# Performance work log

Measured on AMD Instinct MI355X. Metric: run time of the kernel, lower is better.

## Reference

```python
import jax, jax.numpy as jnp
import numpy as np

D_MODEL = 1024
NUM_HEADS = 16


def setup_inputs() -> dict:
    key = jax.random.key(0)
    ks = jax.random.split(key, 5)
    B, S, D = 2, 2048, D_MODEL
    scale = 1.0 / np.sqrt(D)
    return {
        "x": jax.random.normal(ks[0], (B, S, D), dtype=jnp.float32),
        "q_proj_weight": jax.random.normal(ks[1], (D, D), dtype=jnp.float32) * scale,
        "k_proj_weight": jax.random.normal(ks[2], (D, D), dtype=jnp.float32) * scale,
        "v_proj_weight": jax.random.normal(ks[3], (D, D), dtype=jnp.float32) * scale,
        "o_proj_weight": jax.random.normal(ks[4], (D, D), dtype=jnp.float32) * scale,
    }


def _attn(x, qw, kw, vw, ow, num_heads):
    B, S, D = x.shape
    d_k = D // num_heads
    q = x @ qw.T  # [B,S,D]
    k = x @ kw.T
    v = x @ vw.T
    # split heads: [B, H, S, d_k]
    q = q.reshape(B, S, num_heads, d_k).transpose(0, 2, 1, 3)
    k = k.reshape(B, S, num_heads, d_k).transpose(0, 2, 1, 3)
    v = v.reshape(B, S, num_heads, d_k).transpose(0, 2, 1, 3)
    scores = jnp.einsum('bhqd,bhkd->bhqk', q, k) / jnp.sqrt(jnp.asarray(d_k, x.dtype))
    causal = jnp.tril(jnp.ones((S, S), dtype=bool))  # [S,S]
    scores = jnp.where(causal[None, None], scores, jnp.asarray(-jnp.inf, x.dtype))
    attn = jax.nn.softmax(scores, axis=-1)
    out = jnp.einsum('bhqk,bhkd->bhqd', attn, v)  # [B,H,S,d_k]
    out = out.transpose(0, 2, 1, 3).reshape(B, S, D)
    return out @ ow.T


def reference(x, q_proj_weight, k_proj_weight, v_proj_weight, o_proj_weight):
    return _attn(x, q_proj_weight, k_proj_weight, v_proj_weight, o_proj_weight, NUM_HEADS)
```

## Files before the change

kernel.cpp:

```cpp
#include <hip/hip_runtime.h>

typedef __attribute__((ext_vector_type(8))) short short8;
typedef __attribute__((ext_vector_type(4))) float f32x4;

#define MFMA(a,b,c) __builtin_amdgcn_mfma_f32_16x16x32_bf16((a),(b),(c),0,0,0)

#define B_  2
#define S_  2048
#define D_  1024
#define H_  16
#define DK  64
#define KDIM 1024

typedef unsigned int u32;
typedef __attribute__((address_space(1))) const u32 gu32;
typedef __attribute__((address_space(3))) u32 lu32;

__device__ __forceinline__ void gll16(const unsigned short* g, unsigned short* l){
  __builtin_amdgcn_global_load_lds((gu32*)g, (lu32*)l, 16, 0, 0);
}

__device__ __forceinline__ unsigned short f2bf(float f){
  unsigned int u = __float_as_uint(f);
  u += 0x7fffu + ((u >> 16) & 1u);
  return (unsigned short)(u >> 16);
}

__device__ __forceinline__ u32 pkbf(float lo, float hi){
  u32 a = __float_as_uint(lo) + 0x8000u;
  u32 b = __float_as_uint(hi) + 0x8000u;
  return __builtin_amdgcn_perm(b, a, 0x07060302u);
}

__global__ void cvt_all(const float* __restrict__ x,  const float* __restrict__ qw,
                        const float* __restrict__ kw, const float* __restrict__ vw,
                        const float* __restrict__ ow,
                        unsigned short* __restrict__ xb,  unsigned short* __restrict__ wqb,
                        unsigned short* __restrict__ wkb, unsigned short* __restrict__ wvb,
                        unsigned short* __restrict__ wob,
                        int n4x, int n4w){
  int i = blockIdx.x * 256 + threadIdx.x;
  const float* src; unsigned short* dst; int n4;
  switch (blockIdx.y) {
    case 0:  src = x;  dst = xb;  n4 = n4x; break;
    case 1:  src = qw; dst = wqb; n4 = n4w; break;
    case 2:  src = kw; dst = wkb; n4 = n4w; break;
    case 3:  src = vw; dst = wvb; n4 = n4w; break;
    default: src = ow; dst = wob; n4 = n4w; break;
  }
  if (i >= n4) return;
  float4 f = reinterpret_cast<const float4*>(src)[i];
  ushort4 u;
  u.x = f2bf(f.x); u.y = f2bf(f.y); u.z = f2bf(f.z); u.w = f2bf(f.w);
  reinterpret_cast<ushort4*>(dst)[i] = u;
}

__global__ __launch_bounds__(256) void gemm_qkv(
    const unsigned short* __restrict__ X,
    const unsigned short* __restrict__ Wq,
    const unsigned short* __restrict__ Wk,
    const unsigned short* __restrict__ Wv,
    unsigned short* __restrict__ Qo,
    unsigned short* __restrict__ Ko,
    unsigned short* __restrict__ Vo)
{
  const int z = blockIdx.z;
  const unsigned short* __restrict__ W = (z == 0) ? Wq : (z == 1) ? Wk : Wv;
  const int n0 = blockIdx.x * 64;
  const int m0 = blockIdx.y * 128;

  __shared__ unsigned short As0[128 * 32];
  __shared__ unsigned short As1[128 * 32];
  __shared__ unsigned short Bs0[64 * 32];
  __shared__ unsigned short Bs1[64 * 32];

  const int tid  = threadIdx.x;
  const int wid  = tid >> 6, lane = tid & 63;
  const int wm   = (wid >> 1) * 64, wn = (wid & 1) * 32;
  const int lr   = lane & 15, lk = (lane >> 4) * 8;

  const int srow = lane >> 2;
  const int scol = (lane & 3) * 8;
  const unsigned short* gA = X + (size_t)(m0 + wid * 32 + srow) * KDIM + scol;
  const unsigned short* gB = W + (size_t)(n0 + wid * 16 + srow) * KDIM + scol;
  unsigned short* lA0 = &As0[(wid * 32) * 32];
  unsigned short* lA1 = &As1[(wid * 32) * 32];
  unsigned short* lB0 = &Bs0[(wid * 16) * 32];
  unsigned short* lB1 = &Bs1[(wid * 16) * 32];

  f32x4 acc[4][2];
  const f32x4 z4 = {0.f, 0.f, 0.f, 0.f};
  for (int i = 0; i < 4; i++)
    for (int j = 0; j < 2; j++) acc[i][j] = z4;

  for (int k0 = 0; k0 < KDIM; k0 += 64) {
    __syncthreads();
    gll16(gA + k0,                  lA0);
    gll16(gA + 16 * KDIM + k0,      lA0 + 16 * 32);
    gll16(gA + k0 + 32,             lA1);
    gll16(gA + 16 * KDIM + k0 + 32, lA1 + 16 * 32);
    gll16(gB + k0,                  lB0);
    gll16(gB + k0 + 32,             lB1);
    __syncthreads();

    short8 a[4], b[2];
    for (int i = 0; i < 4; i++) a[i] = *(const short8*)&As0[(wm + i * 16 + lr) * 32 + lk];
    for (int j = 0; j < 2; j++) b[j] = *(const short8*)&Bs0[(wn + j * 16 + lr) * 32 + lk];
    if (z == 2) {
      for (int i = 0; i < 4; i++)
        for (int j = 0; j < 2; j++)
          acc[i][j] = MFMA(b[j], a[i], acc[i][j]);
    } else {
      for (int i = 0; i < 4; i++)
        for (int j = 0; j < 2; j++)
          acc[i][j] = MFMA(a[i], b[j], acc[i][j]);
    }
    for (int i = 0; i < 4; i++) a[i] = *(const short8*)&As1[(wm + i * 16 + lr) * 32 + lk];
    for (int j = 0; j < 2; j++) b[j] = *(const short8*)&Bs1[(wn + j * 16 + lr) * 32 + lk];
    if (z == 2) {
      for (int i = 0; i < 4; i++)
        for (int j = 0; j < 2; j++)
          acc[i][j] = MFMA(b[j], a[i], acc[i][j]);
    } else {
      for (int i = 0; i < 4; i++)
        for (int j = 0; j < 2; j++)
          acc[i][j] = MFMA(a[i], b[j], acc[i][j]);
    }
  }

  const int rbase = (lane >> 4) * 4;
  if (z == 2) {
    for (int i = 0; i < 4; i++)
      for (int j = 0; j < 2; j++)
        for (int r = 0; r < 4; r++) {
          int dfull = n0 + wn + j * 16 + rbase + r;
          int sfull = m0 + wm + i * 16 + lr;
          int h = dfull >> 6, d = dfull & 63;
          int bb = sfull >> 11, s = sfull & 2047;
          Vo[(((bb * H_ + h) * DK) + d) * S_ + s] = f2bf(acc[i][j][r]);
        }
  } else {
    for (int i = 0; i < 4; i++)
      for (int j = 0; j < 2; j++)
        for (int r = 0; r < 4; r++) {
          int m = m0 + wm + i * 16 + rbase + r;
          int n = n0 + wn + j * 16 + lr;
          float v = acc[i][j][r];
          int bb = m >> 11, s = m & 2047, h = n >> 6, d = n & 63;
          if (z == 0) {
            v *= 0.18033688f;
            Qo[(((bb * H_ + h) * S_) + s) * DK + d] = f2bf(v);
          } else {
            Ko[(((bb * H_ + h) * S_) + s) * DK + d] = f2bf(v);
          }
        }
  }
}

__global__ __launch_bounds__(512, 4) void attn(
    const unsigned short* __restrict__ Q,
    const unsigned short* __restrict__ K,
    const unsigned short* __restrict__ V,
    unsigned short* __restrict__ O)
{
  const int h = blockIdx.y, b = blockIdx.z;
  const int qt = b ? (15 - blockIdx.x) : blockIdx.x;

  const unsigned short* __restrict__ Qh = Q + (size_t)((b * H_ + h) * S_) * DK;
  const unsigned short* __restrict__ Kh = K + (size_t)((b * H_ + h) * S_) * DK;
  const unsigned short* __restrict__ Vh = V + (size_t)((b * H_ + h) * DK) * S_;

  __shared__ unsigned short Ks[64][72];
  __shared__ unsigned short Vs[64][72];
  __shared__ unsigned short Ps[8][16][72];

  const int tid = threadIdx.x, wid = tid >> 6, lane = tid & 63;
  const int lr = lane & 15, lk = (lane >> 4) * 8;
  const int row4 = (lane >> 4) * 4;
  const int q0 = qt * 128;
  const int qcol = q0 + wid * 16 + lr;
  const int qwmin = q0 + wid * 16;
  const int qwmax = qwmin + 15;
  const int lrow = tid >> 3, lcol = (tid & 7) * 8;

  const short ONE = (short)0x3F80;
  const short8 ones = {ONE, ONE, ONE, ONE, ONE, ONE, ONE, ONE};

  short8 qf[2];
  qf[0] = *(const short8*)&Qh[(q0 + wid * 16 + lr) * DK + lk];
  qf[1] = *(const short8*)&Qh[(q0 + wid * 16 + lr) * DK + 32 + lk];

  const f32x4 z4 = {0.f, 0.f, 0.f, 0.f};
  f32x4 o[4];
  for (int i = 0; i < 4; i++) o[i] = z4;
  f32x4 rs = z4;

  const int kt_end = 2 * qt + 2;

  uint4 kr, vr;
  kr = *(const uint4*)&Kh[lrow * DK + lcol];
  vr = *(const uint4*)&Vh[lrow * S_ + lcol];

  for (int kt = 0; kt < kt_end; kt++) {
    const int k0 = kt * 64;
    __syncthreads();
    *(uint4*)&Ks[lrow][lcol] = kr;
    *(uint4*)&Vs[lrow][lcol] = vr;
    __syncthreads();

    if (kt + 1 < kt_end) {
      const int kn = k0 + 64;
      kr = *(const uint4*)&Kh[(kn + lrow) * DK + lcol];
      vr = *(const uint4*)&Vh[lrow * S_ + kn + lcol];
    }

    if (k0 <= qwmax) {
      f32x4 sc[4];
      for (int nt = 0; nt < 4; nt++) {
        short8 kb0 = *(const short8*)&Ks[nt * 16 + lr][lk];
        short8 kb1 = *(const short8*)&Ks[nt * 16 + lr][32 + lk];
        f32x4 s = MFMA(kb0, qf[0], z4);
        sc[nt] = MFMA(kb1, qf[1], s);
      }

      if (k0 + 63 > qwmin) {
        for (int nt = 0; nt < 4; nt++) {
          int kg = k0 + nt * 16 + row4;
          for (int r = 0; r < 4; r++)
            if (kg + r > qcol) sc[nt][r] = -INFINITY;
        }
      }

      for (int nt = 0; nt < 4; nt++) {
        float p0 = __builtin_amdgcn_exp2f(sc[nt][0]);
        float p1 = __builtin_amdgcn_exp2f(sc[nt][1]);
        float p2 = __builtin_amdgcn_exp2f(sc[nt][2]);
        float p3 = __builtin_amdgcn_exp2f(sc[nt][3]);
        uint2 pk;
        pk.x = pkbf(p0, p1);
        pk.y = pkbf(p2, p3);
        *(uint2*)&Ps[wid][lr][nt * 16 + row4] = pk;
      }

      short8 pf0 = *(const short8*)&Ps[wid][lr][lk];
      short8 pf1 = *(const short8*)&Ps[wid][lr][32 + lk];

      rs = MFMA(ones, pf0, rs);
      rs = MFMA(ones, pf1, rs);

      for (int dt = 0; dt < 4; dt++) {
        short8 vb0 = *(const short8*)&Vs[dt * 16 + lr][lk];
        short8 vb1 = *(const short8*)&Vs[dt * 16 + lr][32 + lk];
        o[dt] = MFMA(vb0, pf0, o[dt]);
        o[dt] = MFMA(vb1, pf1, o[dt]);
      }
    }
  }

  const float inv = 1.0f / rs[0];

  const int srow = q0 + wid * 16 + lr;
  for (int dt = 0; dt < 4; dt++) {
    uint2 pk;
    pk.x = pkbf(o[dt][0] * inv, o[dt][1] * inv);
    pk.y = pkbf(o[dt][2] * inv, o[dt][3] * inv);
    *(uint2*)&O[(size_t)(b * S_ + srow) * D_ + h * DK + dt * 16 + row4] = pk;
  }
}

__global__ __launch_bounds__(256) void gemm_oproj(
    const unsigned short* __restrict__ A,
    const unsigned short* __restrict__ W,
    float* __restrict__ out)
{
  const int n0 = blockIdx.x * 64;
  const int m0 = blockIdx.y * 128;

  __shared__ unsigned short As0[128 * 32];
  __shared__ unsigned short As1[128 * 32];
  __shared__ unsigned short Bs0[64 * 32];
  __shared__ unsigned short Bs1[64 * 32];

  const int tid  = threadIdx.x;
  const int wid  = tid >> 6, lane = tid & 63;
  const int wm   = (wid >> 1) * 64, wn = (wid & 1) * 32;
  const int lr   = lane & 15, lk = (lane >> 4) * 8;

  const int srow = lane >> 2;
  const int scol = (lane & 3) * 8;
  const unsigned short* gA = A + (size_t)(m0 + wid * 32 + srow) * KDIM + scol;
  const unsigned short* gB = W + (size_t)(n0 + wid * 16 + srow) * KDIM + scol;
  unsigned short* lA0 = &As0[(wid * 32) * 32];
  unsigned short* lA1 = &As1[(wid * 32) * 32];
  unsigned short* lB0 = &Bs0[(wid * 16) * 32];
  unsigned short* lB1 = &Bs1[(wid * 16) * 32];

  f32x4 acc[4][2];
  const f32x4 z4 = {0.f, 0.f, 0.f, 0.f};
  for (int i = 0; i < 4; i++)
    for (int j = 0; j < 2; j++) acc[i][j] = z4;

  for (int k0 = 0; k0 < KDIM; k0 += 64) {
    __syncthreads();
    gll16(gA + k0,                  lA0);
    gll16(gA + 16 * KDIM + k0,      lA0 + 16 * 32);
    gll16(gA + k0 + 32,             lA1);
    gll16(gA + 16 * KDIM + k0 + 32, lA1 + 16 * 32);
    gll16(gB + k0,                  lB0);
    gll16(gB + k0 + 32,             lB1);
    __syncthreads();

    short8 a[4], b[2];
    for (int i = 0; i < 4; i++) a[i] = *(const short8*)&As0[(wm + i * 16 + lr) * 32 + lk];
    for (int j = 0; j < 2; j++) b[j] = *(const short8*)&Bs0[(wn + j * 16 + lr) * 32 + lk];
    for (int i = 0; i < 4; i++)
      for (int j = 0; j < 2; j++)
        acc[i][j] = MFMA(a[i], b[j], acc[i][j]);
    for (int i = 0; i < 4; i++) a[i] = *(const short8*)&As1[(wm + i * 16 + lr) * 32 + lk];
    for (int j = 0; j < 2; j++) b[j] = *(const short8*)&Bs1[(wn + j * 16 + lr) * 32 + lk];
    for (int i = 0; i < 4; i++)
      for (int j = 0; j < 2; j++)
        acc[i][j] = MFMA(a[i], b[j], acc[i][j]);
  }

  const int rbase = (lane >> 4) * 4;
  for (int i = 0; i < 4; i++)
    for (int j = 0; j < 2; j++)
      for (int r = 0; r < 4; r++) {
        int m = m0 + wm + i * 16 + rbase + r;
        int n = n0 + wn + j * 16 + lr;
        out[(size_t)m * D_ + n] = acc[i][j][r];
      }
}

extern "C" void kernel_launch(void* const* d_in, const int* in_sizes, int n_in,
                              void* d_out, int out_size, void* d_ws, size_t ws_size,
                              hipStream_t stream) {
  const float* x  = (const float*)d_in[0];
  const float* qw = (const float*)d_in[1];
  const float* kw = (const float*)d_in[2];
  const float* vw = (const float*)d_in[3];
  const float* ow = (const float*)d_in[4];
  float* out = (float*)d_out;

  char* ws = (char*)d_ws;
  size_t off = 0;
  auto alloc = [&](size_t bytes) -> void* {
    void* p = ws + off;
    off += (bytes + 255) & ~(size_t)255;
    return p;
  };
  const size_t XN = (size_t)B_ * S_ * D_;
  const size_t WN = (size_t)D_ * D_;
  unsigned short* xb  = (unsigned short*)alloc(XN * 2);
  unsigned short* wqb = (unsigned short*)alloc(WN * 2);
  unsigned short* wkb = (unsigned short*)alloc(WN * 2);
  unsigned short* wvb = (unsigned short*)alloc(WN * 2);
  unsigned short* wob = (unsigned short*)alloc(WN * 2);
  unsigned short* Qb  = (unsigned short*)alloc(XN * 2);
  unsigned short* Kb  = (unsigned short*)alloc(XN * 2);
  unsigned short* Vb  = (unsigned short*)alloc(XN * 2);
  unsigned short* Ob  = (unsigned short*)alloc(XN * 2);

  cvt_all<<<dim3((XN / 4 + 255) / 256, 5), dim3(256), 0, stream>>>(
      x, qw, kw, vw, ow, xb, wqb, wkb, wvb, wob, (int)(XN / 4), (int)(WN / 4));

  gemm_qkv<<<dim3(D_ / 64, (B_ * S_) / 128, 3), dim3(256), 0, stream>>>(
      xb, wqb, wkb, wvb, Qb, Kb, Vb);

  attn<<<dim3(S_ / 128, H_, B_), dim3(512), 0, stream>>>(Qb, Kb, Vb, Ob);

  gemm_oproj<<<dim3(D_ / 64, (B_ * S_) / 128), dim3(256), 0, stream>>>(Ob, wob, out);
}
```

Before: 177.1 us.

## Double-buffer LDS loads in GEMMs and attention with async global-to-LDS copies

The QKV and output-projection GEMMs now split each K-step into two halves. The load of the next half into the other LDS buffer is issued before computing on the current half, so global-to-LDS copies overlap MFMA work instead of waiting behind a barrier. The attention kernel swaps its register-staged K/V prefetch for direct global_load_lds into double-buffered LDS tiles. It also adds an XOR-like swizzle in place of padding to avoid bank conflicts. This relies on the barrier implicitly waiting for outstanding async LDS loads, which is risky if the compiler does not insert vmcnt waits.

```diff
diff --git a/kernel.cpp b/kernel.cpp
--- a/kernel.cpp
+++ b/kernel.cpp
@@ -93,19 +93,10 @@
   for (int i = 0; i < 4; i++)
     for (int j = 0; j < 2; j++) acc[i][j] = z4;
 
-  for (int k0 = 0; k0 < KDIM; k0 += 64) {
-    __syncthreads();
-    gll16(gA + k0,                  lA0);
-    gll16(gA + 16 * KDIM + k0,      lA0 + 16 * 32);
-    gll16(gA + k0 + 32,             lA1);
-    gll16(gA + 16 * KDIM + k0 + 32, lA1 + 16 * 32);
-    gll16(gB + k0,                  lB0);
-    gll16(gB + k0 + 32,             lB1);
-    __syncthreads();
-
+  auto compute = [&](const unsigned short* AS, const unsigned short* BS){
     short8 a[4], b[2];
-    for (int i = 0; i < 4; i++) a[i] = *(const short8*)&As0[(wm + i * 16 + lr) * 32 + lk];
-    for (int j = 0; j < 2; j++) b[j] = *(const short8*)&Bs0[(wn + j * 16 + lr) * 32 + lk];
+    for (int i = 0; i < 4; i++) a[i] = *(const short8*)&AS[(wm + i * 16 + lr) * 32 + lk];
+    for (int j = 0; j < 2; j++) b[j] = *(const short8*)&BS[(wn + j * 16 + lr) * 32 + lk];
     if (z == 2) {
       for (int i = 0; i < 4; i++)
         for (int j = 0; j < 2; j++)
@@ -115,17 +106,29 @@
         for (int j = 0; j < 2; j++)
           acc[i][j] = MFMA(a[i], b[j], acc[i][j]);
     }
-    for (int i = 0; i < 4; i++) a[i] = *(const short8*)&As1[(wm + i * 16 + lr) * 32 + lk];
-    for (int j = 0; j < 2; j++) b[j] = *(const short8*)&Bs1[(wn + j * 16 + lr) * 32 + lk];
-    if (z == 2) {
-      for (int i = 0; i < 4; i++)
-        for (int j = 0; j < 2; j++)
-          acc[i][j] = MFMA(b[j], a[i], acc[i][j]);
-    } else {
-      for (int i = 0; i < 4; i++)
-        for (int j = 0; j < 2; j++)
-          acc[i][j] = MFMA(a[i], b[j], acc[i][j]);
-    }
+  };
+
+  gll16(gA,             lA0);
+  gll16(gA + 16 * KDIM, lA0 + 16 * 32);
+  gll16(gB,             lB0);
+
+  for (int k0 = 0; k0 < KDIM; k0 += 64) {
+    __syncthreads();
+    {
+      const int kn = k0 + 32;
+      gll16(gA + kn,             lA1);
+      gll16(gA + 16 * KDIM + kn, lA1 + 16 * 32);
+      gll16(gB + kn,             lB1);
+    }
+    compute(As0, Bs0);
+    __syncthreads();
+    if (k0 + 64 < KDIM) {
+      const int kn = k0 + 64;
+      gll16(gA + kn,             lA0);
+      gll16(gA + 16 * KDIM + kn, lA0 + 16 * 32);
+      gll16(gB + kn,             lB0);
+    }
+    compute(As1, Bs1);
   }
 
   const int rbase = (lane >> 4) * 4;
@@ -170,18 +173,34 @@
   const unsigned short* __restrict__ Kh = K + (size_t)((b * H_ + h) * S_) * DK;
   const unsigned short* __restrict__ Vh = V + (size_t)((b * H_ + h) * DK) * S_;
 
-  __shared__ unsigned short Ks[64][72];
-  __shared__ unsigned short Vs[64][72];
+  __shared__ unsigned short Ks0[64 * 64];
+  __shared__ unsigned short Ks1[64 * 64];
+  __shared__ unsigned short Vs0[64 * 64];
+  __shared__ unsigned short Vs1[64 * 64];
   __shared__ unsigned short Ps[8][16][72];
 
   const int tid = threadIdx.x, wid = tid >> 6, lane = tid & 63;
-  const int lr = lane & 15, lk = (lane >> 4) * 8;
+  const int lr = lane & 15;
   const int row4 = (lane >> 4) * 4;
   const int q0 = qt * 128;
   const int qcol = q0 + wid * 16 + lr;
   const int qwmin = q0 + wid * 16;
   const int qwmax = qwmin + 15;
-  const int lrow = tid >> 3, lcol = (tid & 7) * 8;
+  const int lk = (lane >> 4) * 8;
+
+  const int pc0 = (((lane >> 4) + lr) & 7) * 8;
+  const int pc1 = (((lane >> 4) + 4 + lr) & 7) * 8;
+
+  const int sr8 = lane >> 3;
+  const int sc8 = lane & 7;
+  const int sg  = (sc8 - sr8) & 7;
+  const int stRow = wid * 8 + sr8;
+  const unsigned short* gK = Kh + (size_t)stRow * DK + sg * 8;
+  const unsigned short* gV = Vh + (size_t)stRow * S_ + sg * 8;
+  unsigned short* lK0 = &Ks0[wid * 8 * 64];
+  unsigned short* lK1 = &Ks1[wid * 8 * 64];
+  unsigned short* lV0 = &Vs0[wid * 8 * 64];
+  unsigned short* lV1 = &Vs1[wid * 8 * 64];
 
   const short ONE = (short)0x3F80;
   const short8 ones = {ONE, ONE, ONE, ONE, ONE, ONE, ONE, ONE};
@@ -195,66 +214,63 @@
   for (int i = 0; i < 4; i++) o[i] = z4;
   f32x4 rs = z4;
 
+  auto tile = [&](int k0, const unsigned short* KS, const unsigned short* VS){
+    if (k0 > qwmax) return;
+    f32x4 sc[4];
+    for (int nt = 0; nt < 4; nt++) {
+      short8 kb0 = *(const short8*)&KS[(nt * 16 + lr) * 64 + pc0];
+      short8 kb1 = *(const short8*)&KS[(nt * 16 + lr) * 64 + pc1];
+      f32x4 s = MFMA(kb0, qf[0], z4);
+      sc[nt] = MFMA(kb1, qf[1], s);
+    }
+    if (k0 + 63 > qwmin) {
+      for (int nt = 0; nt < 4; nt++) {
+        int kg = k0 + nt * 16 + row4;
+        for (int r = 0; r < 4; r++)
+          if (kg + r > qcol) sc[nt][r] = -INFINITY;
+      }
+    }
+    for (int nt = 0; nt < 4; nt++) {
+      float p0 = __builtin_amdgcn_exp2f(sc[nt][0]);
+      float p1 = __builtin_amdgcn_exp2f(sc[nt][1]);
+      float p2 = __builtin_amdgcn_exp2f(sc[nt][2]);
+      float p3 = __builtin_amdgcn_exp2f(sc[nt][3]);
+      uint2 pk;
+      pk.x = pkbf(p0, p1);
+      pk.y = pkbf(p2, p3);
+      *(uint2*)&Ps[wid][lr][nt * 16 + row4] = pk;
+    }
+    short8 pf0 = *(const short8*)&Ps[wid][lr][lk];
+    short8 pf1 = *(const short8*)&Ps[wid][lr][32 + lk];
+    rs = MFMA(ones, pf0, rs);
+    rs = MFMA(ones, pf1, rs);
+    for (int dt = 0; dt < 4; dt++) {
+      short8 vb0 = *(const short8*)&VS[(dt * 16 + lr) * 64 + pc0];
+      short8 vb1 = *(const short8*)&VS[(dt * 16 + lr) * 64 + pc1];
+      o[dt] = MFMA(vb0, pf0, o[dt]);
+      o[dt] = MFMA(vb1, pf1, o[dt]);
+    }
+  };
+
   const int kt_end = 2 * qt + 2;
 
-  uint4 kr, vr;
-  kr = *(const uint4*)&Kh[lrow * DK + lcol];
-  vr = *(const uint4*)&Vh[lrow * S_ + lcol];
-
-  for (int kt = 0; kt < kt_end; kt++) {
+  gll16(gK, lK0);
+  gll16(gV, lV0);
+
+  for (int kt = 0; kt < kt_end; kt += 2) {
     const int k0 = kt * 64;
     __syncthreads();
-    *(uint4*)&Ks[lrow][lcol] = kr;
-    *(uint4*)&Vs[lrow][lcol] = vr;
-    __syncthreads();
-
-    if (kt + 1 < kt_end) {
-      const int kn = k0 + 64;
-      kr = *(const uint4*)&Kh[(kn + lrow) * DK + lcol];
-      vr = *(const uint4*)&Vh[lrow * S_ + kn + lcol];
-    }
-
-    if (k0 <= qwmax) {
-      f32x4 sc[4];
-      for (int nt = 0; nt < 4; nt++) {
-        short8 kb0 = *(const short8*)&Ks[nt * 16 + lr][lk];
-        short8 kb1 = *(const short8*)&Ks[nt * 16 + lr][32 + lk];
-        f32x4 s = MFMA(kb0, qf[0], z4);
-        sc[nt] = MFMA(kb1, qf[1], s);
-      }
-
-      if (k0 + 63 > qwmin) {
-        for (int nt = 0; nt < 4; nt++) {
-          int kg = k0 + nt * 16 + row4;
-          for (int r = 0; r < 4; r++)
-            if (kg + r > qcol) sc[nt][r] = -INFINITY;
-        }
-      }
-
-      for (int nt = 0; nt < 4; nt++) {
-        float p0 = __builtin_amdgcn_exp2f(sc[nt][0]);
-        float p1 = __builtin_amdgcn_exp2f(sc[nt][1]);
-        float p2 = __builtin_amdgcn_exp2f(sc[nt][2]);
-        float p3 = __builtin_amdgcn_exp2f(sc[nt][3]);
-        uint2 pk;
-        pk.x = pkbf(p0, p1);
-        pk.y = pkbf(p2, p3);
-        *(uint2*)&Ps[wid][lr][nt * 16 + row4] = pk;
-      }
-
-      short8 pf0 = *(const short8*)&Ps[wid][lr][lk];
-      short8 pf1 = *(const short8*)&Ps[wid][lr][32 + lk];
-
-      rs = MFMA(ones, pf0, rs);
-      rs = MFMA(ones, pf1, rs);
-
-      for (int dt = 0; dt < 4; dt++) {
-        short8 vb0 = *(const short8*)&Vs[dt * 16 + lr][lk];
-        short8 vb1 = *(const short8*)&Vs[dt * 16 + lr][32 + lk];
-        o[dt] = MFMA(vb0, pf0, o[dt]);
-        o[dt] = MFMA(vb1, pf1, o[dt]);
-      }
-    }
+    {
+      gll16(gK + (size_t)(k0 + 64) * DK, lK1);
+      gll16(gV + (k0 + 64),              lV1);
+    }
+    tile(k0, Ks0, Vs0);
+    __syncthreads();
+    if (kt + 2 < kt_end) {
+      gll16(gK + (size_t)(k0 + 128) * DK, lK0);
+      gll16(gV + (k0 + 128),              lV0);
+    }
+    tile(k0 + 64, Ks1, Vs1);
   }
 
   const float inv = 1.0f / rs[0];
@@ -300,27 +316,36 @@
   for (int i = 0; i < 4; i++)
     for (int j = 0; j < 2; j++) acc[i][j] = z4;
 
-  for (int k0 = 0; k0 < KDIM; k0 += 64) {
-    __syncthreads();
-    gll16(gA + k0,                  lA0);
-    gll16(gA + 16 * KDIM + k0,      lA0 + 16 * 32);
-    gll16(gA + k0 + 32,             lA1);
-    gll16(gA + 16 * KDIM + k0 + 32, lA1 + 16 * 32);
-    gll16(gB + k0,                  lB0);
-    gll16(gB + k0 + 32,             lB1);
-    __syncthreads();
-
+  auto compute = [&](const unsigned short* AS, const unsigned short* BS){
     short8 a[4], b[2];
-    for (int i = 0; i < 4; i++) a[i] = *(const short8*)&As0[(wm + i * 16 + lr) * 32 + lk];
-    for (int j = 0; j < 2; j++) b[j] = *(const short8*)&Bs0[(wn + j * 16 + lr) * 32 + lk];
+    for (int i = 0; i < 4; i++) a[i] = *(const short8*)&AS[(wm + i * 16 + lr) * 32 + lk];
+    for (int j = 0; j < 2; j++) b[j] = *(const short8*)&BS[(wn + j * 16 + lr) * 32 + lk];
     for (int i = 0; i < 4; i++)
       for (int j = 0; j < 2; j++)
         acc[i][j] = MFMA(a[i], b[j], acc[i][j]);
-    for (int i = 0; i < 4; i++) a[i] = *(const short8*)&As1[(wm + i * 16 + lr) * 32 + lk];
-    for (int j = 0; j < 2; j++) b[j] = *(const short8*)&Bs1[(wn + j * 16 + lr) * 32 + lk];
-    for (int i = 0; i < 4; i++)
-      for (int j = 0; j < 2; j++)
-        acc[i][j] = MFMA(a[i], b[j], acc[i][j]);
+  };
+
+  gll16(gA,             lA0);
+  gll16(gA + 16 * KDIM, lA0 + 16 * 32);
+  gll16(gB,             lB0);
+
+  for (int k0 = 0; k0 < KDIM; k0 += 64) {
+    __syncthreads();
+    {
+      const int kn = k0 + 32;
+      gll16(gA + kn,             lA1);
+      gll16(gA + 16 * KDIM + kn, lA1 + 16 * 32);
+      gll16(gB + kn,             lB1);
+    }
+    compute(As0, Bs0);
+    __syncthreads();
+    if (k0 + 64 < KDIM) {
+      const int kn = k0 + 64;
+      gll16(gA + kn,             lA0);
+      gll16(gA + 16 * KDIM + kn, lA0 + 16 * 32);
+      gll16(gB + kn,             lB0);
+    }
+    compute(As1, Bs1);
   }
 
   const int rbase = (lane >> 4) * 4;
```

Result: no change. 177.4 us (+0.2%).

## Double-buffer attention K/V tiles with direct global-to-LDS loads and swizzled layout

Applied to the files above, without the earlier changes.

The attention kernel used to stage K/V tiles through registers and needed two barriers per tile. It now issues global_load_lds directly into two LDS buffers and processes tiles in pairs, so the next tile's copy overlaps compute with one barrier per tile. The padded 72-column LDS rows are replaced by an unpadded 64-column layout with an XOR-style chunk rotation to avoid bank conflicts. Correctness relies on the barrier implicitly waiting for the async LDS loads, which is a synchronisation risk.

```diff
diff --git a/kernel.cpp b/kernel.cpp
--- a/kernel.cpp
+++ b/kernel.cpp
@@ -170,18 +170,34 @@
   const unsigned short* __restrict__ Kh = K + (size_t)((b * H_ + h) * S_) * DK;
   const unsigned short* __restrict__ Vh = V + (size_t)((b * H_ + h) * DK) * S_;
 
-  __shared__ unsigned short Ks[64][72];
-  __shared__ unsigned short Vs[64][72];
+  __shared__ unsigned short Ks0[64 * 64];
+  __shared__ unsigned short Ks1[64 * 64];
+  __shared__ unsigned short Vs0[64 * 64];
+  __shared__ unsigned short Vs1[64 * 64];
   __shared__ unsigned short Ps[8][16][72];
 
   const int tid = threadIdx.x, wid = tid >> 6, lane = tid & 63;
-  const int lr = lane & 15, lk = (lane >> 4) * 8;
+  const int lr = lane & 15;
   const int row4 = (lane >> 4) * 4;
   const int q0 = qt * 128;
   const int qcol = q0 + wid * 16 + lr;
   const int qwmin = q0 + wid * 16;
   const int qwmax = qwmin + 15;
-  const int lrow = tid >> 3, lcol = (tid & 7) * 8;
+  const int lk = (lane >> 4) * 8;
+
+  const int pc0 = (((lane >> 4) + lr) & 7) * 8;
+  const int pc1 = (((lane >> 4) + 4 + lr) & 7) * 8;
+
+  const int sr8 = lane >> 3;
+  const int sc8 = lane & 7;
+  const int sg  = (sc8 - sr8) & 7;
+  const int stRow = wid * 8 + sr8;
+  const unsigned short* gK = Kh + (size_t)stRow * DK + sg * 8;
+  const unsigned short* gV = Vh + (size_t)stRow * S_ + sg * 8;
+  unsigned short* lK0 = &Ks0[wid * 8 * 64];
+  unsigned short* lK1 = &Ks1[wid * 8 * 64];
+  unsigned short* lV0 = &Vs0[wid * 8 * 64];
+  unsigned short* lV1 = &Vs1[wid * 8 * 64];
 
   const short ONE = (short)0x3F80;
   const short8 ones = {ONE, ONE, ONE, ONE, ONE, ONE, ONE, ONE};
@@ -195,66 +211,63 @@
   for (int i = 0; i < 4; i++) o[i] = z4;
   f32x4 rs = z4;
 
+  auto tile = [&](int k0, const unsigned short* KS, const unsigned short* VS){
+    if (k0 > qwmax) return;
+    f32x4 sc[4];
+    for (int nt = 0; nt < 4; nt++) {
+      short8 kb0 = *(const short8*)&KS[(nt * 16 + lr) * 64 + pc0];
+      short8 kb1 = *(const short8*)&KS[(nt * 16 + lr) * 64 + pc1];
+      f32x4 s = MFMA(kb0, qf[0], z4);
+      sc[nt] = MFMA(kb1, qf[1], s);
+    }
+    if (k0 + 63 > qwmin) {
+      for (int nt = 0; nt < 4; nt++) {
+        int kg = k0 + nt * 16 + row4;
+        for (int r = 0; r < 4; r++)
+          if (kg + r > qcol) sc[nt][r] = -INFINITY;
+      }
+    }
+    for (int nt = 0; nt < 4; nt++) {
+      float p0 = __builtin_amdgcn_exp2f(sc[nt][0]);
+      float p1 = __builtin_amdgcn_exp2f(sc[nt][1]);
+      float p2 = __builtin_amdgcn_exp2f(sc[nt][2]);
+      float p3 = __builtin_amdgcn_exp2f(sc[nt][3]);
+      uint2 pk;
+      pk.x = pkbf(p0, p1);
+      pk.y = pkbf(p2, p3);
+      *(uint2*)&Ps[wid][lr][nt * 16 + row4] = pk;
+    }
+    short8 pf0 = *(const short8*)&Ps[wid][lr][lk];
+    short8 pf1 = *(const short8*)&Ps[wid][lr][32 + lk];
+    rs = MFMA(ones, pf0, rs);
+    rs = MFMA(ones, pf1, rs);
+    for (int dt = 0; dt < 4; dt++) {
+      short8 vb0 = *(const short8*)&VS[(dt * 16 + lr) * 64 + pc0];
+      short8 vb1 = *(const short8*)&VS[(dt * 16 + lr) * 64 + pc1];
+      o[dt] = MFMA(vb0, pf0, o[dt]);
+      o[dt] = MFMA(vb1, pf1, o[dt]);
+    }
+  };
+
   const int kt_end = 2 * qt + 2;
 
-  uint4 kr, vr;
-  kr = *(const uint4*)&Kh[lrow * DK + lcol];
-  vr = *(const uint4*)&Vh[lrow * S_ + lcol];
-
-  for (int kt = 0; kt < kt_end; kt++) {
+  gll16(gK, lK0);
+  gll16(gV, lV0);
+
+  for (int kt = 0; kt < kt_end; kt += 2) {
     const int k0 = kt * 64;
     __syncthreads();
-    *(uint4*)&Ks[lrow][lcol] = kr;
-    *(uint4*)&Vs[lrow][lcol] = vr;
-    __syncthreads();
-
-    if (kt + 1 < kt_end) {
-      const int kn = k0 + 64;
-      kr = *(const uint4*)&Kh[(kn + lrow) * DK + lcol];
-      vr = *(const uint4*)&Vh[lrow * S_ + kn + lcol];
-    }
-
-    if (k0 <= qwmax) {
-      f32x4 sc[4];
-      for (int nt = 0; nt < 4; nt++) {
-        short8 kb0 = *(const short8*)&Ks[nt * 16 + lr][lk];
-        short8 kb1 = *(const short8*)&Ks[nt * 16 + lr][32 + lk];
-        f32x4 s = MFMA(kb0, qf[0], z4);
-        sc[nt] = MFMA(kb1, qf[1], s);
-      }
-
-      if (k0 + 63 > qwmin) {
-        for (int nt = 0; nt < 4; nt++) {
-          int kg = k0 + nt * 16 + row4;
-          for (int r = 0; r < 4; r++)
-            if (kg + r > qcol) sc[nt][r] = -INFINITY;
-        }
-      }
-
-      for (int nt = 0; nt < 4; nt++) {
-        float p0 = __builtin_amdgcn_exp2f(sc[nt][0]);
-        float p1 = __builtin_amdgcn_exp2f(sc[nt][1]);
-        float p2 = __builtin_amdgcn_exp2f(sc[nt][2]);
-        float p3 = __builtin_amdgcn_exp2f(sc[nt][3]);
-        uint2 pk;
-        pk.x = pkbf(p0, p1);
-        pk.y = pkbf(p2, p3);
-        *(uint2*)&Ps[wid][lr][nt * 16 + row4] = pk;
-      }
-
-      short8 pf0 = *(const short8*)&Ps[wid][lr][lk];
-      short8 pf1 = *(const short8*)&Ps[wid][lr][32 + lk];
-
-      rs = MFMA(ones, pf0, rs);
-      rs = MFMA(ones, pf1, rs);
-
-      for (int dt = 0; dt < 4; dt++) {
-        short8 vb0 = *(const short8*)&Vs[dt * 16 + lr][lk];
-        short8 vb1 = *(const short8*)&Vs[dt * 16 + lr][32 + lk];
-        o[dt] = MFMA(vb0, pf0, o[dt]);
-        o[dt] = MFMA(vb1, pf1, o[dt]);
-      }
-    }
+    {
+      gll16(gK + (size_t)(k0 + 64) * DK, lK1);
+      gll16(gV + (k0 + 64),              lV1);
+    }
+    tile(k0, Ks0, Vs0);
+    __syncthreads();
+    if (kt + 2 < kt_end) {
+      gll16(gK + (size_t)(k0 + 128) * DK, lK0);
+      gll16(gV + (k0 + 128),              lV0);
+    }
+    tile(k0 + 64, Ks1, Vs1);
   }
 
   const float inv = 1.0f / rs[0];
```

New measurement: 173.3 us. 2.1% less time.
